# Kernel tuning notes

Hardware: AMD Instinct MI355X
Metric: run time of the kernel (lower is better)

The kernel has to match this reference:

```python
import jax, jax.numpy as jnp
import numpy as np

B, C, M, K, V, D, H, A, L, HF = 2, 128, 4, 4, 64, 1024, 16, 64, 4, 2048
E = M + K
EPS = 1e-5
THETA = 10000.0


def _rmsnorm(x, w):
    return x * jax.lax.rsqrt(jnp.mean(x * x, -1, keepdims=True) + EPS) * w


def _l2norm(x):
    n = jnp.sqrt(jnp.sum(x * x, -1, keepdims=True))
    return x / jnp.maximum(n, EPS)


def _rope(x, cos, sin):
    x1, x2 = jnp.split(x, 2, axis=-1)
    return jnp.concatenate([x1 * cos + x2 * sin, -x1 * sin + x2 * cos], -1)


def _forward(x_input, dec_w1, dec_w2, pos_emb, Wqkv, Wo, Wup, Wdown, attn_norm_w, ffn_norm_w, doc):
    b = x_input.shape[0]
    c = x_input.shape[1] // M
    # decoder_w1 then 'b (c m) (k v) -> b c k (m v)', decoder_w2, pos emb
    x = jnp.einsum('bsd,od->bso', x_input, dec_w1)
    x = x.reshape(b, c, M, K, V).transpose(0, 1, 3, 2, 4).reshape(b, c, K, M * V)
    x = jnp.einsum('bcku,du->bckd', x, dec_w2) + pos_emb
    # decoder_include_original_token: prepend original m tokens per block
    x = jnp.concatenate([x_input.reshape(b, c, M, D), x], axis=2).reshape(b, c * E, D)
    s = c * E
    # mask_mod (decoder_global_original_attn): (causal & kv%e<k & same_doc) | same_block
    idx = jnp.arange(s)
    blk = idx // E
    docs = doc[:, blk]  # [b, s]
    doc_m = docs[:, :, None] == docs[:, None, :]
    causal = blk[:, None] >= blk[None, :]
    kv_ok = (idx % E) < K
    same = blk[:, None] == blk[None, :]
    mask = (causal[None] & kv_ok[None, None, :] & doc_m) | same[None]  # [b, s, s]
    # rotary tables (applied post head-split, dim A)
    inv_freq = (1.0 / THETA) ** (jnp.arange(0, A, 2) / A)
    freqs = jnp.arange(s)[:, None] * inv_freq[None, :]
    cos, sin = jnp.cos(freqs), jnp.sin(freqs)  # [s, A/2]
    scale = 1.0 / jnp.sqrt(jnp.float32(A))
    neg = jnp.float32(-1e30)

    def heads(t):
        return t.reshape(b, s, H, A).transpose(0, 2, 1, 3)

    for li in range(L):
        xn = _rmsnorm(x, attn_norm_w[li])
        qkv = jnp.einsum('bsd,od->bso', xn, Wqkv[li])
        q, k, v = jnp.split(qkv, 3, axis=-1)
        q, k, v = heads(q), heads(k), heads(v)
        q, k = _l2norm(q), _l2norm(k)  # qk_norm
        q, k = _rope(q, cos, sin), _rope(k, cos, sin)
        scores = jnp.einsum('bhqa,bhka->bhqk', q, k) * scale
        scores = jnp.where(mask[:, None], scores, neg)
        probs = jax.nn.softmax(scores, axis=-1)
        attn = jnp.einsum('bhqk,bhka->bhqa', probs, v)
        attn = attn.transpose(0, 2, 1, 3).reshape(b, s, D)
        x1_in = jnp.einsum('bsd,od->bso', attn, Wo[li]) + x
        xf = _rmsnorm(x1_in, ffn_norm_w[li])
        up = jnp.einsum('bsd,od->bso', xf, Wup[li])
        u1, u2 = jnp.split(up, 2, axis=-1)
        x = jnp.einsum('bsh,dh->bsd', jax.nn.silu(u1) * u2, Wdown[li]) + x1_in
    # 'b (c e) d -> (b c) e d' then drop original tokens
    return x.reshape(b * c, E, D)[:, M:]


def setup_inputs() -> dict:
    key = jax.random.key(0)
    ks = jax.random.split(key, 10)
    sc = 0.02
    return {
        'x_input': jax.random.normal(ks[0], (B, C * M, D), jnp.float32),
        'doc': jnp.sort(jax.random.randint(ks[1], (B, C), 0, 4), axis=-1),
        'dec_w1': jax.random.normal(ks[2], (K * V, D), jnp.float32) * sc,
        'dec_w2': jax.random.normal(ks[3], (D, M * V), jnp.float32) * sc,
        'pos_emb': jax.random.normal(ks[4], (1, 1, K, D), jnp.float32) * sc,
        'Wqkv': jax.random.normal(ks[5], (L, 3 * D, D), jnp.float32) * sc,
        'Wo': jax.random.normal(ks[6], (L, D, D), jnp.float32) * sc,
        'Wup': jax.random.normal(ks[7], (L, 2 * HF, D), jnp.float32) * sc,
        'Wdown': jax.random.normal(ks[8], (L, D, HF), jnp.float32) * sc,
        'attn_norm_w': jnp.ones((L, D), jnp.float32),
        'ffn_norm_w': jnp.ones((L, D), jnp.float32),
    }


def reference(x_input, doc, dec_w1, dec_w2, pos_emb, Wqkv, Wo, Wup, Wdown, attn_norm_w, ffn_norm_w):
    return _forward(x_input, dec_w1, dec_w2, pos_emb, Wqkv, Wo, Wup, Wdown, attn_norm_w, ffn_norm_w, doc)
```

## Files before the change

kernel.cpp:

```cpp
#include <hip/hip_runtime.h>
#include <hip/hip_bf16.h>

typedef __bf16 bf16;
typedef __bf16 bf16x8 __attribute__((ext_vector_type(8)));
typedef __bf16 bf16x4 __attribute__((ext_vector_type(4)));
typedef float  f32x4  __attribute__((ext_vector_type(4)));

#define MFMA16(a, b, c) __builtin_amdgcn_mfma_f32_16x16x32_bf16(a, b, c, 0, 0, 0)

template <int EPI, int AF32, int BF32, int TM, int TN, int SK = 1>
__global__ __launch_bounds__(256 * SK) void gemm_bt(
    const void* __restrict__ Av, const void* __restrict__ Bv,
    const float* __restrict__ Res, void* __restrict__ Out,
    int Ntot, int Ktot, int lda)
{
    constexpr int PA = TM / 64, PB = TN / 64;
    constexpr int WN = (TN == 128) ? ((TM == 128) ? 2 : 4) : 2;
    constexpr int WM = 4 / WN;
    constexpr int I = TM / (WM * 16), J = TN / (WN * 16);
    __shared__ __align__(16) bf16 As[2][SK][TM][40];
    __shared__ __align__(16) bf16 Bs[2][SK][TN][40];
    static_assert(SK == 1 || sizeof(As) >= TM * TN * 4, "combine buffer fits in As");
    const int tid  = threadIdx.x;
    const int grp  = (SK > 1) ? (tid >> 8) : 0;
    const int t8   = tid & 255;
    const int wave = t8 >> 6, lane = tid & 63;
    const int quad = lane >> 4, l16 = lane & 15;
    const int wm = wave / WN, wn = wave % WN;
    const int rowW = wm * (TM / WM), colW = wn * (TN / WN);
    const int rowBase = blockIdx.y * TM, colBase = blockIdx.x * TN;

    f32x4 acc[I][J];
    const f32x4 z4 = {0.f, 0.f, 0.f, 0.f};
#pragma unroll
    for (int i = 0; i < I; i++)
#pragma unroll
        for (int j = 0; j < J; j++) acc[i][j] = z4;

    float4 rAf[PA][2]; bf16x8 rAb[PA];
    float4 rBf[PB][2]; bf16x8 rBb[PB];

    auto loadTile = [&](int kt) {
#pragma unroll
        for (int p = 0; p < PA; p++) {
            int ch = p * 256 + t8, r = ch >> 2, c8 = (ch & 3) << 3;
            if (AF32) {
                const float* s = (const float*)Av + (size_t)(rowBase + r) * lda + kt + c8;
                rAf[p][0] = *(const float4*)s; rAf[p][1] = *(const float4*)(s + 4);
            } else {
                rAb[p] = *(const bf16x8*)((const bf16*)Av + (size_t)(rowBase + r) * lda + kt + c8);
            }
        }
#pragma unroll
        for (int p = 0; p < PB; p++) {
            int ch = p * 256 + t8, r = ch >> 2, c8 = (ch & 3) << 3;
            if (BF32) {
                const float* s = (const float*)Bv + (size_t)(colBase + r) * Ktot + kt + c8;
                rBf[p][0] = *(const float4*)s; rBf[p][1] = *(const float4*)(s + 4);
            } else {
                rBb[p] = *(const bf16x8*)((const bf16*)Bv + (size_t)(colBase + r) * Ktot + kt + c8);
            }
        }
    };
    auto storeTile = [&](int buf) {
#pragma unroll
        for (int p = 0; p < PA; p++) {
            int ch = p * 256 + t8, r = ch >> 2, c8 = (ch & 3) << 3;
            bf16x8 t;
            if (AF32) {
                t[0]=(bf16)rAf[p][0].x; t[1]=(bf16)rAf[p][0].y; t[2]=(bf16)rAf[p][0].z; t[3]=(bf16)rAf[p][0].w;
                t[4]=(bf16)rAf[p][1].x; t[5]=(bf16)rAf[p][1].y; t[6]=(bf16)rAf[p][1].z; t[7]=(bf16)rAf[p][1].w;
            } else t = rAb[p];
            *(bf16x8*)&As[buf][grp][r][c8] = t;
        }
#pragma unroll
        for (int p = 0; p < PB; p++) {
            int ch = p * 256 + t8, r = ch >> 2, c8 = (ch & 3) << 3;
            bf16x8 t;
            if (BF32) {
                t[0]=(bf16)rBf[p][0].x; t[1]=(bf16)rBf[p][0].y; t[2]=(bf16)rBf[p][0].z; t[3]=(bf16)rBf[p][0].w;
                t[4]=(bf16)rBf[p][1].x; t[5]=(bf16)rBf[p][1].y; t[6]=(bf16)rBf[p][1].z; t[7]=(bf16)rBf[p][1].w;
            } else t = rBb[p];
            *(bf16x8*)&Bs[buf][grp][r][c8] = t;
        }
    };

    const int Kgrp  = Ktot / SK;
    const int kbase = grp * Kgrp;
    loadTile(kbase);
    storeTile(0);
    __syncthreads();
    const int nk = Kgrp >> 5;
    for (int k = 0; k < nk; k++) {
        const bool more = (k + 1) < nk;
        if (more) loadTile(kbase + ((k + 1) << 5));
        const int buf = k & 1;
        bf16x8 af[I], bfr[J];
#pragma unroll
        for (int i = 0; i < I; i++)
            af[i] = *(const bf16x8*)&As[buf][grp][rowW + i * 16 + l16][quad * 8];
#pragma unroll
        for (int j = 0; j < J; j++)
            bfr[j] = *(const bf16x8*)&Bs[buf][grp][colW + j * 16 + l16][quad * 8];
#pragma unroll
        for (int i = 0; i < I; i++)
#pragma unroll
            for (int j = 0; j < J; j++)
                acc[i][j] = MFMA16(af[i], bfr[j], acc[i][j]);
        if (more) { storeTile(buf ^ 1); __syncthreads(); }
    }

    if (SK == 2) {
        __syncthreads();
        float* red = (float*)&As[0][0][0][0];
        if (grp == 1) {
#pragma unroll
            for (int i = 0; i < I; i++)
#pragma unroll
                for (int j = 0; j < J; j++)
#pragma unroll
                    for (int r = 0; r < 4; r++)
                        red[(rowW + i * 16 + quad * 4 + r) * TN +
                            (colW + j * 16 + l16)] = acc[i][j][r];
        }
        __syncthreads();
        if (grp != 0) return;
#pragma unroll
        for (int i = 0; i < I; i++)
#pragma unroll
            for (int j = 0; j < J; j++)
#pragma unroll
                for (int r = 0; r < 4; r++)
                    acc[i][j][r] += red[(rowW + i * 16 + quad * 4 + r) * TN +
                                        (colW + j * 16 + l16)];
    }

#pragma unroll
    for (int i = 0; i < I; i++) {
        int row0 = rowBase + rowW + i * 16 + quad * 4;
#pragma unroll
        for (int j = 0; j < J; j++) {
            int col = colBase + colW + j * 16 + l16;
#pragma unroll
            for (int r = 0; r < 4; r++) {
                size_t off = (size_t)(row0 + r) * Ntot + col;
                float v = acc[i][j][r];
                if (EPI == 0)      ((bf16*)Out)[off]  = (bf16)v;
                else if (EPI == 1) ((float*)Out)[off] = v + Res[off];
                else               ((float*)Out)[off] = v;
            }
        }
    }
}

__global__ __launch_bounds__(256) void gemm_up_swiglu(
    const bf16* __restrict__ A, const float* __restrict__ B,
    bf16* __restrict__ Out)
{
    __shared__ __align__(16) bf16 As[2][128][40];
    __shared__ __align__(16) bf16 Bs[2][128][40];
    const int tid  = threadIdx.x;
    const int wave = tid >> 6, lane = tid & 63;
    const int quad = lane >> 4, l16 = lane & 15;
    const int wm = wave >> 1, wn = wave & 1;
    const int rowBase = blockIdx.y * 128, cb = blockIdx.x;

    f32x4 acc[4][4];
    const f32x4 z4 = {0.f, 0.f, 0.f, 0.f};
#pragma unroll
    for (int i = 0; i < 4; i++)
#pragma unroll
        for (int j = 0; j < 4; j++) acc[i][j] = z4;

    bf16x8 rA[2]; float4 rB[2][2];
    auto loadTile = [&](int kt) {
#pragma unroll
        for (int p = 0; p < 2; p++) {
            int ch = p * 256 + tid, r = ch >> 2, c8 = (ch & 3) << 3;
            rA[p] = *(const bf16x8*)(A + (size_t)(rowBase + r) * 1024 + kt + c8);
            int brow = (r >> 6) * 2048 + cb * 64 + (r & 63);
            const float* s = B + (size_t)brow * 1024 + kt + c8;
            rB[p][0] = *(const float4*)s; rB[p][1] = *(const float4*)(s + 4);
        }
    };
    auto storeTile = [&](int buf) {
#pragma unroll
        for (int p = 0; p < 2; p++) {
            int ch = p * 256 + tid, r = ch >> 2, c8 = (ch & 3) << 3;
            *(bf16x8*)&As[buf][r][c8] = rA[p];
            bf16x8 t;
            t[0]=(bf16)rB[p][0].x; t[1]=(bf16)rB[p][0].y; t[2]=(bf16)rB[p][0].z; t[3]=(bf16)rB[p][0].w;
            t[4]=(bf16)rB[p][1].x; t[5]=(bf16)rB[p][1].y; t[6]=(bf16)rB[p][1].z; t[7]=(bf16)rB[p][1].w;
            *(bf16x8*)&Bs[buf][r][c8] = t;
        }
    };

    loadTile(0);
    storeTile(0);
    __syncthreads();
    for (int k = 0; k < 32; k++) {
        const bool more = k < 31;
        if (more) loadTile((k + 1) << 5);
        const int buf = k & 1;
        bf16x8 af[4], bfr[4];
#pragma unroll
        for (int i = 0; i < 4; i++)
            af[i] = *(const bf16x8*)&As[buf][wm * 64 + i * 16 + l16][quad * 8];
#pragma unroll
        for (int j = 0; j < 4; j++) {
            int brow = (j < 2) ? (wn * 32 + j * 16) : (64 + wn * 32 + (j - 2) * 16);
            bfr[j] = *(const bf16x8*)&Bs[buf][brow + l16][quad * 8];
        }
#pragma unroll
        for (int i = 0; i < 4; i++)
#pragma unroll
            for (int j = 0; j < 4; j++)
                acc[i][j] = MFMA16(af[i], bfr[j], acc[i][j]);
        if (more) { storeTile(buf ^ 1); __syncthreads(); }
    }

#pragma unroll
    for (int i = 0; i < 4; i++) {
        int row0 = rowBase + wm * 64 + i * 16 + quad * 4;
#pragma unroll
        for (int jj = 0; jj < 2; jj++) {
            int col = cb * 64 + wn * 32 + jj * 16 + l16;
#pragma unroll
            for (int r = 0; r < 4; r++) {
                float u1 = acc[i][jj][r], u2 = acc[i][jj + 2][r];
                float g = u1 / (1.f + __expf(-u1));
                Out[(size_t)(row0 + r) * 2048 + col] = (bf16)(g * u2);
            }
        }
    }
}

__global__ __launch_bounds__(256) void rmsnorm_k(
    const float* __restrict__ X, const float* __restrict__ W,
    bf16* __restrict__ Out)
{
    const int row = blockIdx.x, tid = threadIdx.x;
    const float4 xv = *(const float4*)(X + (size_t)row * 1024 + tid * 4);
    float ss = xv.x * xv.x + xv.y * xv.y + xv.z * xv.z + xv.w * xv.w;
#pragma unroll
    for (int m = 1; m < 64; m <<= 1) ss += __shfl_xor(ss, m);
    __shared__ float red[4];
    if ((tid & 63) == 0) red[tid >> 6] = ss;
    __syncthreads();
    float tot = red[0] + red[1] + red[2] + red[3];
    float sc = rsqrtf(tot * (1.0f / 1024.0f) + 1e-5f);
    const float4 wv = *(const float4*)(W + tid * 4);
    bf16x4 o;
    o[0] = (bf16)(xv.x * sc * wv.x);
    o[1] = (bf16)(xv.y * sc * wv.y);
    o[2] = (bf16)(xv.z * sc * wv.z);
    o[3] = (bf16)(xv.w * sc * wv.w);
    *(bf16x4*)(Out + (size_t)row * 1024 + tid * 4) = o;
}

__global__ __launch_bounds__(256) void ropetab_k(float* __restrict__ tab)
{
    int i = blockIdx.x * 256 + threadIdx.x;
    int s = i >> 5, j = i & 31;
    float f = (float)s * __expf(-(float)j * 0.2878231366242557f);
    tab[i * 2]     = cosf(f);
    tab[i * 2 + 1] = sinf(f);
}

__global__ __launch_bounds__(256) void qkprep_k(
    bf16* __restrict__ qkv, const float* __restrict__ tab)
{
    int wid  = blockIdx.x * 4 + (threadIdx.x >> 6);
    int lane = threadIdx.x & 63;
    int s = wid & 1023, h = (wid >> 10) & 15, b = (wid >> 14) & 1, op = wid >> 15;
    bf16* addr = qkv + ((size_t)(b * 1024 + s)) * 3072 + op * 1024 + h * 64 + lane;
    float v = (float)*addr;
    float ss = v * v;
#pragma unroll
    for (int m = 1; m < 64; m <<= 1) ss += __shfl_xor(ss, m);
    v /= fmaxf(sqrtf(ss), 1e-5f);
    float2 cssn = ((const float2*)tab)[(s << 5) + (lane & 31)];
    float partner = __shfl_xor(v, 32);
    float o = (lane < 32) ? (v * cssn.x + partner * cssn.y)
                          : (v * cssn.x - partner * cssn.y);
    if (op == 0) o *= 0.125f;
    *addr = (bf16)o;
}

__global__ __launch_bounds__(256) void vtrans_k(
    const bf16* __restrict__ qkv, bf16* __restrict__ Vt)
{
    __shared__ __align__(16) bf16 Ls[64][72];
    const int st = blockIdx.x, h = blockIdx.y, b = blockIdx.z;
    const int tid = threadIdx.x;
#pragma unroll
    for (int p = 0; p < 2; p++) {
        int s = p * 32 + (tid >> 3), a0 = (tid & 7) << 3;
        *(bf16x8*)&Ls[s][a0] = *(const bf16x8*)(
            qkv + ((size_t)(b * 1024 + st * 64 + s)) * 3072 + 2048 + h * 64 + a0);
    }
    __syncthreads();
#pragma unroll
    for (int p = 0; p < 2; p++) {
        int a = p * 32 + (tid >> 3), s0 = (tid & 7) << 3;
        bf16x8 v;
#pragma unroll
        for (int j = 0; j < 8; j++) v[j] = Ls[s0 + j][a];
        *(bf16x8*)(Vt + (((size_t)((b * 16 + h) * 64 + a)) << 10) + st * 64 + s0) = v;
    }
}

__global__ __launch_bounds__(256) void attn_k(
    const bf16* __restrict__ qkv, const bf16* __restrict__ Vt,
    const int* __restrict__ doc, bf16* __restrict__ attnb)
{
    const int p = blockIdx.x, h = blockIdx.y, b = blockIdx.z;
    const int tid = threadIdx.x, w = tid >> 6, lane = tid & 63;
    const int quad = lane >> 4, l16 = lane & 15;
    __shared__ __align__(16) bf16 PsT[4][64][20];
    __shared__ int docL[128];
    if (tid < 128) docL[tid] = doc[b * 128 + tid];
    __syncthreads();

    const int g = (w == 0) ? p : (w == 1) ? 31 - p : (w == 2) ? 32 + p : 63 - p;
    const bf16* qp = qkv + ((size_t)(b * 1024 + g * 16 + l16)) * 3072 + h * 64 + quad * 8;
    const bf16x8 qf0 = *(const bf16x8*)qp;
    const bf16x8 qf1 = *(const bf16x8*)(qp + 32);
    const bf16* Kbase = qkv + ((size_t)(b * 1024)) * 3072 + 1024 + h * 64;
    const bf16* Vbase = Vt + (((size_t)((b * 16 + h) * 64)) << 10);

    const f32x4 z4 = {0.f, 0.f, 0.f, 0.f};
    f32x4 O[4] = {z4, z4, z4, z4};
    float lp[4] = {0.f, 0.f, 0.f, 0.f};

    int bq[4], dq[4];
#pragma unroll
    for (int r = 0; r < 4; r++) {
        bq[r] = (g * 16 + quad * 4 + r) >> 3;
        dq[r] = docL[bq[r]];
    }

    bf16x8 kc[8], kn[8];
    auto loadK = [&](int kt, bf16x8* dst) {
        const bf16* kp = Kbase + (size_t)(kt * 64 + l16) * 3072 + quad * 8;
#pragma unroll
        for (int kg = 0; kg < 4; kg++) {
            dst[kg * 2]     = *(const bf16x8*)(kp + (size_t)kg * 16 * 3072);
            dst[kg * 2 + 1] = *(const bf16x8*)(kp + (size_t)kg * 16 * 3072 + 32);
        }
    };

    const int tiles = (g + 4) >> 2;
    loadK(0, kc);
    for (int kt = 0; kt < tiles; kt++) {
        const int k0 = kt * 64;
        f32x4 sf[4];
#pragma unroll
        for (int kg = 0; kg < 4; kg++) {
            sf[kg] = z4;
            sf[kg] = MFMA16(qf0, kc[kg * 2],     sf[kg]);
            sf[kg] = MFMA16(qf1, kc[kg * 2 + 1], sf[kg]);
        }
        bf16x8 vr[4][2];
#pragma unroll
        for (int t = 0; t < 4; t++)
#pragma unroll
            for (int c = 0; c < 2; c++)
                vr[t][c] = *(const bf16x8*)(
                    Vbase + ((size_t)(t * 16 + l16) << 10) + k0 + c * 32 + quad * 8);
        if (kt + 1 < tiles) loadK(kt + 1, kn);

        float pvv[4][4];
#pragma unroll
        for (int kg = 0; kg < 4; kg++) {
            int kgi = k0 + kg * 16 + l16;
            int bk  = kgi >> 3;
            int dkv = docL[bk];
            bool kbit = (kgi & 7) < 4;
#pragma unroll
            for (int r = 0; r < 4; r++) {
                bool ok = (bq[r] == bk) || ((bq[r] >= bk) && kbit && (dq[r] == dkv));
                float pp = ok ? __expf(sf[kg][r]) : 0.f;
                pvv[kg][r] = pp;
                lp[r] += pp;
            }
        }
#pragma unroll
        for (int kg = 0; kg < 4; kg++) {
            bf16x4 t4;
#pragma unroll
            for (int r = 0; r < 4; r++) t4[r] = (bf16)pvv[kg][r];
            *(bf16x4*)&PsT[w][kg * 16 + l16][quad * 4] = t4;
        }
        bf16x8 pa0, pa1;
#pragma unroll
        for (int j = 0; j < 8; j++) {
            pa0[j] = PsT[w][quad * 8 + j][l16];
            pa1[j] = PsT[w][32 + quad * 8 + j][l16];
        }
#pragma unroll
        for (int t = 0; t < 4; t++) {
            O[t] = MFMA16(pa0, vr[t][0], O[t]);
            O[t] = MFMA16(pa1, vr[t][1], O[t]);
        }
        if (kt + 1 < tiles) {
#pragma unroll
            for (int i = 0; i < 8; i++) kc[i] = kn[i];
        }
    }

#pragma unroll
    for (int r = 0; r < 4; r++) {
#pragma unroll
        for (int m = 1; m < 16; m <<= 1) lp[r] += __shfl_xor(lp[r], m);
    }

#pragma unroll
    for (int t = 0; t < 4; t++)
#pragma unroll
        for (int r = 0; r < 4; r++) {
            int qg = g * 16 + quad * 4 + r;
            float v = O[t][r] / fmaxf(lp[r], 1e-20f);
            attnb[((size_t)(b * 1024) + qg) * 1024 + h * 64 + t * 16 + l16] = (bf16)v;
        }
}

__global__ __launch_bounds__(256) void permute_k(
    const bf16* __restrict__ t1, bf16* __restrict__ t1p)
{
    int idx = blockIdx.x * 256 + threadIdx.x;
    int u = idx & 255, m = u >> 6, v = u & 63;
    int orow = idx >> 8;
    int k = orow & 3, bc = orow >> 2;
    int b = bc >> 7, c = bc & 127;
    t1p[idx] = t1[((size_t)(b * 512 + c * 4 + m)) * 256 + k * 64 + v];
}

__global__ __launch_bounds__(256) void buildx_k(
    const float* __restrict__ x_input, const float* __restrict__ t2,
    const float* __restrict__ pos_emb, float* __restrict__ xres)
{
    int idx = blockIdx.x * 256 + threadIdx.x;
    int d = idx & 1023, row = idx >> 10;
    int b = row >> 10, rr = row & 1023;
    int c = rr >> 3, e = rr & 7;
    float v;
    if (e < 4)
        v = x_input[((size_t)(b * 512 + c * 4 + e)) * 1024 + d];
    else
        v = t2[((size_t)(b * 512 + c * 4 + (e - 4))) * 1024 + d] +
            pos_emb[(e - 4) * 1024 + d];
    xres[idx] = v;
}

__global__ __launch_bounds__(256) void finalout_k(
    const float* __restrict__ xres, float* __restrict__ out)
{
    int idx = blockIdx.x * 256 + threadIdx.x;
    int d = idx & 1023, t = idx >> 10;
    int kk = t & 3, bc = t >> 2;
    int b = bc >> 7, c = bc & 127;
    out[idx] = xres[((size_t)(b * 1024 + c * 8 + 4 + kk)) * 1024 + d];
}

extern "C" void kernel_launch(void* const* d_in, const int* in_sizes, int n_in,
                              void* d_out, int out_size, void* d_ws, size_t ws_size,
                              hipStream_t stream)
{
    const float* x_input = (const float*)d_in[0];
    const int*   doc     = (const int*)d_in[1];
    const float* dec_w1  = (const float*)d_in[2];
    const float* dec_w2  = (const float*)d_in[3];
    const float* pos_emb = (const float*)d_in[4];
    const float* Wqkv    = (const float*)d_in[5];
    const float* Wo      = (const float*)d_in[6];
    const float* Wup     = (const float*)d_in[7];
    const float* Wdown   = (const float*)d_in[8];
    const float* anw     = (const float*)d_in[9];
    const float* fnw     = (const float*)d_in[10];
    float* out = (float*)d_out;

    char* w = (char*)d_ws;
    float* xres  = (float*)(w);
    bf16*  attnb = (bf16*)(w + (8u << 20));
    bf16*  t1    = (bf16*)(w + (8u << 20));
    bf16*  t1p   = (bf16*)(w + (8u << 20) + (512u << 10));
    bf16*  Vt    = (bf16*)(w + (12u << 20));
    bf16*  xn2   = (bf16*)(w + (12u << 20));
    bf16*  qkv   = (bf16*)(w + (16u << 20));
    float* t2    = (float*)(w + (16u << 20));
    float* x1res = (float*)(w + (16u << 20));
    bf16*  hg    = (bf16*)(w + (24u << 20));
    bf16*  xn1   = (bf16*)(w + (28u << 20));
    float* rtab  = out;

    ropetab_k<<<128, 256, 0, stream>>>(rtab);
    gemm_bt<0, 1, 1, 64, 64><<<dim3(4, 16), 256, 0, stream>>>(
        x_input, dec_w1, nullptr, t1, 256, 1024, 1024);
    permute_k<<<1024, 256, 0, stream>>>(t1, t1p);
    gemm_bt<2, 0, 1, 64, 64><<<dim3(16, 16), 256, 0, stream>>>(
        t1p, dec_w2, nullptr, t2, 1024, 256, 256);
    buildx_k<<<8192, 256, 0, stream>>>(x_input, t2, pos_emb, xres);

    for (int li = 0; li < 4; ++li) {
        rmsnorm_k<<<2048, 256, 0, stream>>>(xres, anw + li * 1024, xn1);
        gemm_bt<0, 0, 1, 128, 128><<<dim3(24, 16), 256, 0, stream>>>(
            xn1, Wqkv + (size_t)li * 3072 * 1024, nullptr, qkv, 3072, 1024, 1024);
        qkprep_k<<<16384, 256, 0, stream>>>(qkv, rtab);
        vtrans_k<<<dim3(16, 16, 2), 256, 0, stream>>>(qkv, Vt);
        attn_k<<<dim3(16, 16, 2), 256, 0, stream>>>(qkv, Vt, doc, attnb);
        gemm_bt<1, 0, 1, 64, 64, 2><<<dim3(16, 32), 512, 0, stream>>>(
            attnb, Wo + (size_t)li * 1024 * 1024, xres, x1res, 1024, 1024, 1024);
        rmsnorm_k<<<2048, 256, 0, stream>>>(x1res, fnw + li * 1024, xn2);
        gemm_up_swiglu<<<dim3(32, 16), 256, 0, stream>>>(
            xn2, Wup + (size_t)li * 4096 * 1024, hg);
        gemm_bt<1, 0, 1, 64, 64, 2><<<dim3(16, 32), 512, 0, stream>>>(
            hg, Wdown + (size_t)li * 1024 * 2048, x1res, xres, 1024, 2048, 2048);
    }

    finalout_k<<<4096, 256, 0, stream>>>(xres, out);
}
```

Baseline: 891.6 us.

## Split K dimension across two wave groups in SwiGLU up-GEMM and attention

Result: no change. 902.1 us (+1.2%).

```diff
diff --git a/kernel.cpp b/kernel.cpp
--- a/kernel.cpp
+++ b/kernel.cpp
@@ -153,14 +153,14 @@
     }
 }
 
-__global__ __launch_bounds__(256) void gemm_up_swiglu(
+__global__ __launch_bounds__(512) void gemm_up_swiglu(
     const bf16* __restrict__ A, const float* __restrict__ B,
     bf16* __restrict__ Out)
 {
-    __shared__ __align__(16) bf16 As[2][128][40];
-    __shared__ __align__(16) bf16 Bs[2][128][40];
+    __shared__ __align__(16) bf16 Smem[2][2][256][40];
     const int tid  = threadIdx.x;
-    const int wave = tid >> 6, lane = tid & 63;
+    const int grp  = tid >> 8, t8 = tid & 255;
+    const int wave = t8 >> 6, lane = tid & 63;
     const int quad = lane >> 4, l16 = lane & 15;
     const int wm = wave >> 1, wn = wave & 1;
     const int rowBase = blockIdx.y * 128, cb = blockIdx.x;
@@ -176,7 +176,7 @@
     auto loadTile = [&](int kt) {
 #pragma unroll
         for (int p = 0; p < 2; p++) {
-            int ch = p * 256 + tid, r = ch >> 2, c8 = (ch & 3) << 3;
+            int ch = p * 256 + t8, r = ch >> 2, c8 = (ch & 3) << 3;
             rA[p] = *(const bf16x8*)(A + (size_t)(rowBase + r) * 1024 + kt + c8);
             int brow = (r >> 6) * 2048 + cb * 64 + (r & 63);
             const float* s = B + (size_t)brow * 1024 + kt + c8;
@@ -186,30 +186,31 @@
     auto storeTile = [&](int buf) {
 #pragma unroll
         for (int p = 0; p < 2; p++) {
-            int ch = p * 256 + tid, r = ch >> 2, c8 = (ch & 3) << 3;
-            *(bf16x8*)&As[buf][r][c8] = rA[p];
+            int ch = p * 256 + t8, r = ch >> 2, c8 = (ch & 3) << 3;
+            *(bf16x8*)&Smem[buf][grp][r][c8] = rA[p];
             bf16x8 t;
             t[0]=(bf16)rB[p][0].x; t[1]=(bf16)rB[p][0].y; t[2]=(bf16)rB[p][0].z; t[3]=(bf16)rB[p][0].w;
             t[4]=(bf16)rB[p][1].x; t[5]=(bf16)rB[p][1].y; t[6]=(bf16)rB[p][1].z; t[7]=(bf16)rB[p][1].w;
-            *(bf16x8*)&Bs[buf][r][c8] = t;
+            *(bf16x8*)&Smem[buf][grp][128 + r][c8] = t;
         }
     };
 
-    loadTile(0);
+    const int kbase = grp * 512;
+    loadTile(kbase);
     storeTile(0);
     __syncthreads();
-    for (int k = 0; k < 32; k++) {
-        const bool more = k < 31;
-        if (more) loadTile((k + 1) << 5);
+    for (int k = 0; k < 16; k++) {
+        const bool more = k < 15;
+        if (more) loadTile(kbase + ((k + 1) << 5));
         const int buf = k & 1;
         bf16x8 af[4], bfr[4];
 #pragma unroll
         for (int i = 0; i < 4; i++)
-            af[i] = *(const bf16x8*)&As[buf][wm * 64 + i * 16 + l16][quad * 8];
+            af[i] = *(const bf16x8*)&Smem[buf][grp][wm * 64 + i * 16 + l16][quad * 8];
 #pragma unroll
         for (int j = 0; j < 4; j++) {
             int brow = (j < 2) ? (wn * 32 + j * 16) : (64 + wn * 32 + (j - 2) * 16);
-            bfr[j] = *(const bf16x8*)&Bs[buf][brow + l16][quad * 8];
+            bfr[j] = *(const bf16x8*)&Smem[buf][grp][128 + brow + l16][quad * 8];
         }
 #pragma unroll
         for (int i = 0; i < 4; i++)
@@ -218,6 +219,33 @@
                 acc[i][j] = MFMA16(af[i], bfr[j], acc[i][j]);
         if (more) { storeTile(buf ^ 1); __syncthreads(); }
     }
+
+    __syncthreads();
+    float* red = (float*)&Smem[0][0][0][0];
+    if (grp == 1) {
+#pragma unroll
+        for (int i = 0; i < 4; i++)
+#pragma unroll
+            for (int j = 0; j < 4; j++) {
+                int brow = ((j < 2) ? (wn * 32 + j * 16)
+                                    : (64 + wn * 32 + (j - 2) * 16)) + l16;
+#pragma unroll
+                for (int r = 0; r < 4; r++)
+                    red[(wm * 64 + i * 16 + quad * 4 + r) * 128 + brow] = acc[i][j][r];
+            }
+    }
+    __syncthreads();
+    if (grp != 0) return;
+#pragma unroll
+    for (int i = 0; i < 4; i++)
+#pragma unroll
+        for (int j = 0; j < 4; j++) {
+            int brow = ((j < 2) ? (wn * 32 + j * 16)
+                                : (64 + wn * 32 + (j - 2) * 16)) + l16;
+#pragma unroll
+            for (int r = 0; r < 4; r++)
+                acc[i][j][r] += red[(wm * 64 + i * 16 + quad * 4 + r) * 128 + brow];
+        }
 
 #pragma unroll
     for (int i = 0; i < 4; i++) {
@@ -310,14 +338,16 @@
     }
 }
 
-__global__ __launch_bounds__(256) void attn_k(
+__global__ __launch_bounds__(512) void attn_k(
     const bf16* __restrict__ qkv, const bf16* __restrict__ Vt,
     const int* __restrict__ doc, bf16* __restrict__ attnb)
 {
     const int p = blockIdx.x, h = blockIdx.y, b = blockIdx.z;
-    const int tid = threadIdx.x, w = tid >> 6, lane = tid & 63;
+    const int tid = threadIdx.x, w8 = tid >> 6, lane = tid & 63;
+    const int w = w8 & 3, half = w8 >> 2;
     const int quad = lane >> 4, l16 = lane & 15;
-    __shared__ __align__(16) bf16 PsT[4][64][20];
+    __shared__ __align__(16) bf16 PsT[8][64][20];
+    __shared__ float cmb[4][64][20];
     __shared__ int docL[128];
     if (tid < 128) docL[tid] = doc[b * 128 + tid];
     __syncthreads();
@@ -350,64 +380,87 @@
         }
     };
 
-    const int tiles = (g + 4) >> 2;
-    loadK(0, kc);
-    for (int kt = 0; kt < tiles; kt++) {
-        const int k0 = kt * 64;
-        f32x4 sf[4];
-#pragma unroll
-        for (int kg = 0; kg < 4; kg++) {
-            sf[kg] = z4;
-            sf[kg] = MFMA16(qf0, kc[kg * 2],     sf[kg]);
-            sf[kg] = MFMA16(qf1, kc[kg * 2 + 1], sf[kg]);
-        }
-        bf16x8 vr[4][2];
+    const int T   = (g + 4) >> 2;
+    const int Th  = (T + 1) >> 1;
+    const int kt0 = half ? Th : 0;
+    const int kt1 = half ? T  : Th;
+
+    if (kt0 < kt1) {
+        loadK(kt0, kc);
+        for (int kt = kt0; kt < kt1; kt++) {
+            const int k0 = kt * 64;
+            f32x4 sf[4];
+#pragma unroll
+            for (int kg = 0; kg < 4; kg++) {
+                sf[kg] = z4;
+                sf[kg] = MFMA16(qf0, kc[kg * 2],     sf[kg]);
+                sf[kg] = MFMA16(qf1, kc[kg * 2 + 1], sf[kg]);
+            }
+            bf16x8 vr[4][2];
+#pragma unroll
+            for (int t = 0; t < 4; t++)
+#pragma unroll
+                for (int c = 0; c < 2; c++)
+                    vr[t][c] = *(const bf16x8*)(
+                        Vbase + ((size_t)(t * 16 + l16) << 10) + k0 + c * 32 + quad * 8);
+            if (kt + 1 < kt1) loadK(kt + 1, kn);
+
+            float pvv[4][4];
+#pragma unroll
+            for (int kg = 0; kg < 4; kg++) {
+                int kgi = k0 + kg * 16 + l16;
+                int bk  = kgi >> 3;
+                int dkv = docL[bk];
+                bool kbit = (kgi & 7) < 4;
+#pragma unroll
+                for (int r = 0; r < 4; r++) {
+                    bool ok = (bq[r] == bk) || ((bq[r] >= bk) && kbit && (dq[r] == dkv));
+                    float pp = ok ? __expf(sf[kg][r]) : 0.f;
+                    pvv[kg][r] = pp;
+                    lp[r] += pp;
+                }
+            }
+#pragma unroll
+            for (int kg = 0; kg < 4; kg++) {
+                bf16x4 t4;
+#pragma unroll
+                for (int r = 0; r < 4; r++) t4[r] = (bf16)pvv[kg][r];
+                *(bf16x4*)&PsT[w8][kg * 16 + l16][quad * 4] = t4;
+            }
+            bf16x8 pa0, pa1;
+#pragma unroll
+            for (int j = 0; j < 8; j++) {
+                pa0[j] = PsT[w8][quad * 8 + j][l16];
+                pa1[j] = PsT[w8][32 + quad * 8 + j][l16];
+            }
+#pragma unroll
+            for (int t = 0; t < 4; t++) {
+                O[t] = MFMA16(pa0, vr[t][0], O[t]);
+                O[t] = MFMA16(pa1, vr[t][1], O[t]);
+            }
+            if (kt + 1 < kt1) {
+#pragma unroll
+                for (int i = 0; i < 8; i++) kc[i] = kn[i];
+            }
+        }
+    }
+
+    if (half) {
 #pragma unroll
         for (int t = 0; t < 4; t++)
 #pragma unroll
-            for (int c = 0; c < 2; c++)
-                vr[t][c] = *(const bf16x8*)(
-                    Vbase + ((size_t)(t * 16 + l16) << 10) + k0 + c * 32 + quad * 8);
-        if (kt + 1 < tiles) loadK(kt + 1, kn);
-
-        float pvv[4][4];
-#pragma unroll
-        for (int kg = 0; kg < 4; kg++) {
-            int kgi = k0 + kg * 16 + l16;
-            int bk  = kgi >> 3;
-            int dkv = docL[bk];
-            bool kbit = (kgi & 7) < 4;
-#pragma unroll
-            for (int r = 0; r < 4; r++) {
-                bool ok = (bq[r] == bk) || ((bq[r] >= bk) && kbit && (dq[r] == dkv));
-                float pp = ok ? __expf(sf[kg][r]) : 0.f;
-                pvv[kg][r] = pp;
-                lp[r] += pp;
-            }
-        }
-#pragma unroll
-        for (int kg = 0; kg < 4; kg++) {
-            bf16x4 t4;
-#pragma unroll
-            for (int r = 0; r < 4; r++) t4[r] = (bf16)pvv[kg][r];
-            *(bf16x4*)&PsT[w][kg * 16 + l16][quad * 4] = t4;
-        }
-        bf16x8 pa0, pa1;
-#pragma unroll
-        for (int j = 0; j < 8; j++) {
-            pa0[j] = PsT[w][quad * 8 + j][l16];
-            pa1[j] = PsT[w][32 + quad * 8 + j][l16];
-        }
-#pragma unroll
-        for (int t = 0; t < 4; t++) {
-            O[t] = MFMA16(pa0, vr[t][0], O[t]);
-            O[t] = MFMA16(pa1, vr[t][1], O[t]);
-        }
-        if (kt + 1 < tiles) {
-#pragma unroll
-            for (int i = 0; i < 8; i++) kc[i] = kn[i];
-        }
-    }
+            for (int r = 0; r < 4; r++) cmb[w][lane][t * 4 + r] = O[t][r];
+#pragma unroll
+        for (int r = 0; r < 4; r++) cmb[w][lane][16 + r] = lp[r];
+    }
+    __syncthreads();
+    if (half) return;
+#pragma unroll
+    for (int t = 0; t < 4; t++)
+#pragma unroll
+        for (int r = 0; r < 4; r++) O[t][r] += cmb[w][lane][t * 4 + r];
+#pragma unroll
+    for (int r = 0; r < 4; r++) lp[r] += cmb[w][lane][16 + r];
 
 #pragma unroll
     for (int r = 0; r < 4; r++) {
@@ -508,11 +561,11 @@
             xn1, Wqkv + (size_t)li * 3072 * 1024, nullptr, qkv, 3072, 1024, 1024);
         qkprep_k<<<16384, 256, 0, stream>>>(qkv, rtab);
         vtrans_k<<<dim3(16, 16, 2), 256, 0, stream>>>(qkv, Vt);
-        attn_k<<<dim3(16, 16, 2), 256, 0, stream>>>(qkv, Vt, doc, attnb);
+        attn_k<<<dim3(16, 16, 2), 512, 0, stream>>>(qkv, Vt, doc, attnb);
         gemm_bt<1, 0, 1, 64, 64, 2><<<dim3(16, 32), 512, 0, stream>>>(
             attnb, Wo + (size_t)li * 1024 * 1024, xres, x1res, 1024, 1024, 1024);
         rmsnorm_k<<<2048, 256, 0, stream>>>(x1res, fnw + li * 1024, xn2);
-        gemm_up_swiglu<<<dim3(32, 16), 256, 0, stream>>>(
+        gemm_up_swiglu<<<dim3(32, 16), 512, 0, stream>>>(
             xn2, Wup + (size_t)li * 4096 * 1024, hg);
         gemm_bt<1, 0, 1, 64, 64, 2><<<dim3(16, 32), 512, 0, stream>>>(
             hg, Wdown + (size_t)li * 1024 * 2048, x1res, xres, 1024, 2048, 2048);
```

## Share K/V tiles via double-buffered LDS in paired-block attention, fuse prep kernels

Applied to the files above, without the earlier changes.

After: 895.4 us. No clear change (+0.4%).

```diff
diff --git a/kernel.cpp b/kernel.cpp
--- a/kernel.cpp
+++ b/kernel.cpp
@@ -11,7 +11,7 @@
 template <int EPI, int AF32, int BF32, int TM, int TN, int SK = 1>
 __global__ __launch_bounds__(256 * SK) void gemm_bt(
     const void* __restrict__ Av, const void* __restrict__ Bv,
-    const float* __restrict__ Res, void* __restrict__ Out,
+    const float* Res, void* Out,
     int Ntot, int Ktot, int lda)
 {
     constexpr int PA = TM / 64, PB = TN / 64;
@@ -267,62 +267,67 @@
     tab[i * 2 + 1] = sinf(f);
 }
 
-__global__ __launch_bounds__(256) void qkprep_k(
-    bf16* __restrict__ qkv, const float* __restrict__ tab)
-{
-    int wid  = blockIdx.x * 4 + (threadIdx.x >> 6);
-    int lane = threadIdx.x & 63;
-    int s = wid & 1023, h = (wid >> 10) & 15, b = (wid >> 14) & 1, op = wid >> 15;
-    bf16* addr = qkv + ((size_t)(b * 1024 + s)) * 3072 + op * 1024 + h * 64 + lane;
-    float v = (float)*addr;
-    float ss = v * v;
-#pragma unroll
-    for (int m = 1; m < 64; m <<= 1) ss += __shfl_xor(ss, m);
-    v /= fmaxf(sqrtf(ss), 1e-5f);
-    float2 cssn = ((const float2*)tab)[(s << 5) + (lane & 31)];
-    float partner = __shfl_xor(v, 32);
-    float o = (lane < 32) ? (v * cssn.x + partner * cssn.y)
-                          : (v * cssn.x - partner * cssn.y);
-    if (op == 0) o *= 0.125f;
-    *addr = (bf16)o;
-}
-
-__global__ __launch_bounds__(256) void vtrans_k(
-    const bf16* __restrict__ qkv, bf16* __restrict__ Vt)
+__global__ __launch_bounds__(256) void qkvprep_k(
+    bf16* __restrict__ qkv, const float* __restrict__ tab,
+    bf16* __restrict__ Vt)
 {
     __shared__ __align__(16) bf16 Ls[64][72];
-    const int st = blockIdx.x, h = blockIdx.y, b = blockIdx.z;
     const int tid = threadIdx.x;
-#pragma unroll
-    for (int p = 0; p < 2; p++) {
-        int s = p * 32 + (tid >> 3), a0 = (tid & 7) << 3;
-        *(bf16x8*)&Ls[s][a0] = *(const bf16x8*)(
-            qkv + ((size_t)(b * 1024 + st * 64 + s)) * 3072 + 2048 + h * 64 + a0);
-    }
-    __syncthreads();
-#pragma unroll
-    for (int p = 0; p < 2; p++) {
-        int a = p * 32 + (tid >> 3), s0 = (tid & 7) << 3;
-        bf16x8 v;
-#pragma unroll
-        for (int j = 0; j < 8; j++) v[j] = Ls[s0 + j][a];
-        *(bf16x8*)(Vt + (((size_t)((b * 16 + h) * 64 + a)) << 10) + st * 64 + s0) = v;
-    }
-}
-
-__global__ __launch_bounds__(256) void attn_k(
+    if (blockIdx.x < 16384) {
+        int wid  = blockIdx.x * 4 + (tid >> 6);
+        int lane = tid & 63;
+        int s = wid & 1023, h = (wid >> 10) & 15, b = (wid >> 14) & 1, op = wid >> 15;
+        bf16* addr = qkv + ((size_t)(b * 1024 + s)) * 3072 + op * 1024 + h * 64 + lane;
+        float v = (float)*addr;
+        float ss = v * v;
+#pragma unroll
+        for (int m = 1; m < 64; m <<= 1) ss += __shfl_xor(ss, m);
+        v /= fmaxf(sqrtf(ss), 1e-5f);
+        float2 cssn = ((const float2*)tab)[(s << 5) + (lane & 31)];
+        float partner = __shfl_xor(v, 32);
+        float o = (lane < 32) ? (v * cssn.x + partner * cssn.y)
+                              : (v * cssn.x - partner * cssn.y);
+        if (op == 0) o *= 0.125f;
+        *addr = (bf16)o;
+    } else {
+        int id = blockIdx.x - 16384;
+        int st = id & 15, h = (id >> 4) & 15, b = id >> 8;
+#pragma unroll
+        for (int p = 0; p < 2; p++) {
+            int s = p * 32 + (tid >> 3), a0 = (tid & 7) << 3;
+            *(bf16x8*)&Ls[s][a0] = *(const bf16x8*)(
+                qkv + ((size_t)(b * 1024 + st * 64 + s)) * 3072 + 2048 + h * 64 + a0);
+        }
+        __syncthreads();
+#pragma unroll
+        for (int p = 0; p < 2; p++) {
+            int a = p * 32 + (tid >> 3), s0 = (tid & 7) << 3;
+            bf16x8 v;
+#pragma unroll
+            for (int j = 0; j < 8; j++) v[j] = Ls[s0 + j][a];
+            *(bf16x8*)(Vt + (((size_t)((b * 16 + h) * 64 + a)) << 10) + st * 64 + s0) = v;
+        }
+    }
+}
+
+__global__ __launch_bounds__(512) void attn_pair(
     const bf16* __restrict__ qkv, const bf16* __restrict__ Vt,
     const int* __restrict__ doc, bf16* __restrict__ attnb)
 {
-    const int p = blockIdx.x, h = blockIdx.y, b = blockIdx.z;
-    const int tid = threadIdx.x, w = tid >> 6, lane = tid & 63;
+    const int pidx = blockIdx.x, h = blockIdx.y, b = blockIdx.z;
+    const int tid = threadIdx.x, w8 = tid >> 6, lane = tid & 63;
     const int quad = lane >> 4, l16 = lane & 15;
-    __shared__ __align__(16) bf16 PsT[4][64][20];
+    __shared__ __align__(16) bf16 Ks[2][64][72];
+    __shared__ __align__(16) bf16 Vs[2][64][72];
+    __shared__ __align__(16) bf16 PsT[8][64][20];
     __shared__ int docL[128];
     if (tid < 128) docL[tid] = doc[b * 128 + tid];
-    __syncthreads();
-
-    const int g = (w == 0) ? p : (w == 1) ? 31 - p : (w == 2) ? 32 + p : 63 - p;
+
+    const int pgrp = (w8 >= 4) ? (15 - pidx) : pidx;
+    const int g  = 4 * pgrp + (w8 & 3);
+    const int Tw = pgrp + 1;
+    const int Tstage = 16 - pidx;
+
     const bf16* qp = qkv + ((size_t)(b * 1024 + g * 16 + l16)) * 3072 + h * 64 + quad * 8;
     const bf16x8 qf0 = *(const bf16x8*)qp;
     const bf16x8 qf1 = *(const bf16x8*)(qp + 32);
@@ -333,6 +338,21 @@
     f32x4 O[4] = {z4, z4, z4, z4};
     float lp[4] = {0.f, 0.f, 0.f, 0.f};
 
+    bf16x8 rK, rV;
+    auto stageRegs = [&](int kt) {
+        int r = tid >> 3, c8 = (tid & 7) << 3;
+        rK = *(const bf16x8*)(Kbase + (size_t)(kt * 64 + r) * 3072 + c8);
+        rV = *(const bf16x8*)(Vbase + ((size_t)r << 10) + kt * 64 + c8);
+    };
+    auto stageLDS = [&](int buf) {
+        int r = tid >> 3, c8 = (tid & 7) << 3;
+        *(bf16x8*)&Ks[buf][r][c8] = rK;
+        *(bf16x8*)&Vs[buf][r][c8] = rV;
+    };
+
+    stageRegs(0);
+    stageLDS(0);
+    __syncthreads();
     int bq[4], dq[4];
 #pragma unroll
     for (int r = 0; r < 4; r++) {
@@ -340,73 +360,59 @@
         dq[r] = docL[bq[r]];
     }
 
-    bf16x8 kc[8], kn[8];
-    auto loadK = [&](int kt, bf16x8* dst) {
-        const bf16* kp = Kbase + (size_t)(kt * 64 + l16) * 3072 + quad * 8;
-#pragma unroll
-        for (int kg = 0; kg < 4; kg++) {
-            dst[kg * 2]     = *(const bf16x8*)(kp + (size_t)kg * 16 * 3072);
-            dst[kg * 2 + 1] = *(const bf16x8*)(kp + (size_t)kg * 16 * 3072 + 32);
-        }
-    };
-
-    const int tiles = (g + 4) >> 2;
-    loadK(0, kc);
-    for (int kt = 0; kt < tiles; kt++) {
-        const int k0 = kt * 64;
-        f32x4 sf[4];
-#pragma unroll
-        for (int kg = 0; kg < 4; kg++) {
-            sf[kg] = z4;
-            sf[kg] = MFMA16(qf0, kc[kg * 2],     sf[kg]);
-            sf[kg] = MFMA16(qf1, kc[kg * 2 + 1], sf[kg]);
-        }
-        bf16x8 vr[4][2];
-#pragma unroll
-        for (int t = 0; t < 4; t++)
-#pragma unroll
-            for (int c = 0; c < 2; c++)
-                vr[t][c] = *(const bf16x8*)(
-                    Vbase + ((size_t)(t * 16 + l16) << 10) + k0 + c * 32 + quad * 8);
-        if (kt + 1 < tiles) loadK(kt + 1, kn);
-
-        float pvv[4][4];
-#pragma unroll
-        for (int kg = 0; kg < 4; kg++) {
-            int kgi = k0 + kg * 16 + l16;
-            int bk  = kgi >> 3;
-            int dkv = docL[bk];
-            bool kbit = (kgi & 7) < 4;
-#pragma unroll
-            for (int r = 0; r < 4; r++) {
-                bool ok = (bq[r] == bk) || ((bq[r] >= bk) && kbit && (dq[r] == dkv));
-                float pp = ok ? __expf(sf[kg][r]) : 0.f;
-                pvv[kg][r] = pp;
-                lp[r] += pp;
-            }
-        }
-#pragma unroll
-        for (int kg = 0; kg < 4; kg++) {
-            bf16x4 t4;
-#pragma unroll
-            for (int r = 0; r < 4; r++) t4[r] = (bf16)pvv[kg][r];
-            *(bf16x4*)&PsT[w][kg * 16 + l16][quad * 4] = t4;
-        }
-        bf16x8 pa0, pa1;
-#pragma unroll
-        for (int j = 0; j < 8; j++) {
-            pa0[j] = PsT[w][quad * 8 + j][l16];
-            pa1[j] = PsT[w][32 + quad * 8 + j][l16];
-        }
-#pragma unroll
-        for (int t = 0; t < 4; t++) {
-            O[t] = MFMA16(pa0, vr[t][0], O[t]);
-            O[t] = MFMA16(pa1, vr[t][1], O[t]);
-        }
-        if (kt + 1 < tiles) {
-#pragma unroll
-            for (int i = 0; i < 8; i++) kc[i] = kn[i];
-        }
+    for (int kt = 0; kt < Tstage; kt++) {
+        const bool more = (kt + 1) < Tstage;
+        if (more) stageRegs(kt + 1);
+        const int buf = kt & 1;
+        if (kt < Tw) {
+            const int k0 = kt * 64;
+            f32x4 sf[4];
+#pragma unroll
+            for (int kg = 0; kg < 4; kg++) {
+                const bf16x8 k0f = *(const bf16x8*)&Ks[buf][kg * 16 + l16][quad * 8];
+                const bf16x8 k1f = *(const bf16x8*)&Ks[buf][kg * 16 + l16][32 + quad * 8];
+                sf[kg] = z4;
+                sf[kg] = MFMA16(qf0, k0f, sf[kg]);
+                sf[kg] = MFMA16(qf1, k1f, sf[kg]);
+            }
+            float pvv[4][4];
+#pragma unroll
+            for (int kg = 0; kg < 4; kg++) {
+                int kgi = k0 + kg * 16 + l16;
+                int bk  = kgi >> 3;
+                int dkv = docL[bk];
+                bool kbit = (kgi & 7) < 4;
+#pragma unroll
+                for (int r = 0; r < 4; r++) {
+                    bool ok = (bq[r] == bk) || ((bq[r] >= bk) && kbit && (dq[r] == dkv));
+                    float pp = ok ? __expf(sf[kg][r]) : 0.f;
+                    pvv[kg][r] = pp;
+                    lp[r] += pp;
+                }
+            }
+#pragma unroll
+            for (int kg = 0; kg < 4; kg++) {
+                bf16x4 t4;
+#pragma unroll
+                for (int r = 0; r < 4; r++) t4[r] = (bf16)pvv[kg][r];
+                *(bf16x4*)&PsT[w8][kg * 16 + l16][quad * 4] = t4;
+            }
+            bf16x8 pa0, pa1;
+#pragma unroll
+            for (int j = 0; j < 8; j++) {
+                pa0[j] = PsT[w8][quad * 8 + j][l16];
+                pa1[j] = PsT[w8][32 + quad * 8 + j][l16];
+            }
+#pragma unroll
+            for (int t = 0; t < 4; t++) {
+                const bf16x8 v0f = *(const bf16x8*)&Vs[buf][t * 16 + l16][quad * 8];
+                const bf16x8 v1f = *(const bf16x8*)&Vs[buf][t * 16 + l16][32 + quad * 8];
+                O[t] = MFMA16(pa0, v0f, O[t]);
+                O[t] = MFMA16(pa1, v1f, O[t]);
+            }
+        }
+        if (more) stageLDS(buf ^ 1);
+        __syncthreads();
     }
 
 #pragma unroll
@@ -489,7 +495,6 @@
     bf16*  xn2   = (bf16*)(w + (12u << 20));
     bf16*  qkv   = (bf16*)(w + (16u << 20));
     float* t2    = (float*)(w + (16u << 20));
-    float* x1res = (float*)(w + (16u << 20));
     bf16*  hg    = (bf16*)(w + (24u << 20));
     bf16*  xn1   = (bf16*)(w + (28u << 20));
     float* rtab  = out;
@@ -506,16 +511,15 @@
         rmsnorm_k<<<2048, 256, 0, stream>>>(xres, anw + li * 1024, xn1);
         gemm_bt<0, 0, 1, 128, 128><<<dim3(24, 16), 256, 0, stream>>>(
             xn1, Wqkv + (size_t)li * 3072 * 1024, nullptr, qkv, 3072, 1024, 1024);
-        qkprep_k<<<16384, 256, 0, stream>>>(qkv, rtab);
-        vtrans_k<<<dim3(16, 16, 2), 256, 0, stream>>>(qkv, Vt);
-        attn_k<<<dim3(16, 16, 2), 256, 0, stream>>>(qkv, Vt, doc, attnb);
+        qkvprep_k<<<16896, 256, 0, stream>>>(qkv, rtab, Vt);
+        attn_pair<<<dim3(8, 16, 2), 512, 0, stream>>>(qkv, Vt, doc, attnb);
         gemm_bt<1, 0, 1, 64, 64, 2><<<dim3(16, 32), 512, 0, stream>>>(
-            attnb, Wo + (size_t)li * 1024 * 1024, xres, x1res, 1024, 1024, 1024);
-        rmsnorm_k<<<2048, 256, 0, stream>>>(x1res, fnw + li * 1024, xn2);
+            attnb, Wo + (size_t)li * 1024 * 1024, xres, xres, 1024, 1024, 1024);
+        rmsnorm_k<<<2048, 256, 0, stream>>>(xres, fnw + li * 1024, xn2);
         gemm_up_swiglu<<<dim3(32, 16), 256, 0, stream>>>(
             xn2, Wup + (size_t)li * 4096 * 1024, hg);
         gemm_bt<1, 0, 1, 64, 64, 2><<<dim3(16, 32), 512, 0, stream>>>(
-            hg, Wdown + (size_t)li * 1024 * 2048, x1res, xres, 1024, 2048, 2048);
+            hg, Wdown + (size_t)li * 1024 * 2048, xres, xres, 1024, 2048, 2048);
     }
 
     finalout_k<<<4096, 256, 0, stream>>>(xres, out);
```
